# Optimization experiments

Hardware: AMD Instinct MI355X
Metric: run time of the kernel (lower is better)

The kernel has to match this reference:

```python
import jax, jax.numpy as jnp
import numpy as np

NUM_ITERS = 5
EPS = 1e-5


def setup_inputs() -> dict:
    key = jax.random.key(0)
    ks = jax.random.split(key, 5)
    C_in, C_out, D, H, W = 64, 64, 64, 256, 256
    return {
        "x": jax.random.normal(ks[0], (C_in, H, W), dtype=jnp.float32),
        "conv_w": jax.random.normal(ks[1], (C_out, C_in, 3, 3), dtype=jnp.float32) * 0.05,
        "conv_b": jax.random.normal(ks[2], (C_out,), dtype=jnp.float32) * 0.05,
        "bin_proj": jax.random.normal(ks[3], (C_out, D, 1), dtype=jnp.float32),
        "weight_matrix": jax.random.normal(ks[4], (C_out, D, D), dtype=jnp.float32),
        "gn_weight": jnp.ones((C_out,), dtype=jnp.float32),
        "gn_bias": jnp.zeros((C_out,), dtype=jnp.float32),
    }


def reference(x, conv_w, conv_b, bin_proj, weight_matrix, gn_weight, gn_bias):
    # query conv: (C_in,H,W) -> (C_out,H,W), SAME padding
    q = jax.lax.conv_general_dilated(
        x[None], conv_w, window_strides=(1, 1), padding="SAME",
        dimension_numbers=("NCHW", "OIHW", "NCHW"))[0]
    q = q + conv_b[:, None, None]

    bp = bin_proj[:, :, 0]  # (C, D) == bin_proj_c[:, 0] per channel
    # binary query / initial state: (C, H, W, D)
    state = jnp.sign(q[:, :, :, None] * bp[:, None, None, :])
    # unrolled Hopfield dynamics: state = sign(W_c @ state) per channel/pixel
    for _ in range(NUM_ITERS):
        state = jnp.sign(jnp.einsum("cde,chwe->chwd", weight_matrix, state))
    # readout: sum_d bp[c,d] * state[c,h,w,d] -> (C,H,W)
    out = jnp.einsum("cd,chwd->chw", bp, state)

    # GroupNorm(groups=1) over (C,H,W) with per-channel affine, then residual input is out+q
    y = out + q
    mean = jnp.mean(y)
    var = jnp.mean(jnp.square(y - mean))
    yn = (y - mean) * jax.lax.rsqrt(var + EPS)
    yn = yn * gn_weight[:, None, None] + gn_bias[:, None, None]
    return jax.nn.gelu(yn)
```

## Files before the change

kernel.cpp:

```cpp
#include <hip/hip_runtime.h>
#include <math.h>

#define N_TOT 4194304
#define CONV_BLOCKS 1024
#define XS_PAD 4864

__device__ __forceinline__ float sgnf(float x) {
    return x > 0.f ? 1.f : (x < 0.f ? -1.f : 0.f);
}

__device__ __forceinline__ float gelu_f(float v) {
    const float c0 = 0.7978845608028654f;
    float inner = c0 * fmaf(0.044715f * v, v * v, v);
    return 0.5f * v * (1.f + tanhf(inner));
}

__device__ __forceinline__ void gll4(const float* g, float* l) {
    __builtin_amdgcn_global_load_lds((const __attribute__((address_space(1))) void*)g,
                                     (__attribute__((address_space(3))) void*)l, 4, 0, 0);
}

__global__ __launch_bounds__(64) void alpha_kernel(const float* __restrict__ bp,
                                                   const float* __restrict__ Wm,
                                                   float* __restrict__ alpha) {
    const int c = blockIdx.x, d = threadIdx.x;
    __shared__ float v[64];
    float bpv = bp[c * 64 + d];
    v[d] = sgnf(bpv);
    __syncthreads();
    const float* row = Wm + c * 4096 + d * 64;
    for (int it = 0; it < 5; ++it) {
        float s = 0.f;
        #pragma unroll
        for (int e = 0; e < 64; ++e) s = fmaf(row[e], v[e], s);
        __syncthreads();
        v[d] = sgnf(s);
        __syncthreads();
    }
    float val = bpv * v[d];
    #pragma unroll
    for (int off = 32; off; off >>= 1) val += __shfl_down(val, off);
    if (d == 0) alpha[c] = val;
}

__global__ __launch_bounds__(256, 4) void conv_kernel(const float* __restrict__ x,
                                                      const float* __restrict__ cw,
                                                      const float* __restrict__ cb,
                                                      const float* __restrict__ alpha,
                                                      const float* __restrict__ zbuf,
                                                      float* __restrict__ y,
                                                      double* __restrict__ partials) {
    const int tid = threadIdx.x;
    const int b = blockIdx.x;
    const int tile = b & 63;
    const int cog = b >> 6;
    const int bx = tile & 7, by = tile >> 3;
    const int tx = tid & 15, ty = tid >> 4;
    const int x0 = (bx << 5) - 1, y0 = (by << 5) - 1;

    __shared__ float xs[2][XS_PAD];
    __shared__ double red[4][2];

    int voff[19];
    unsigned vmask = 0u;
    #pragma unroll
    for (int i = 0; i < 19; ++i) {
        int idx = i * 256 + tid;
        int r = idx / 136;
        int rem = idx - r * 136;
        int ci = rem / 34;
        int c = rem - ci * 34;
        int gy = y0 + r, gx = x0 + c;
        bool ok = (idx < 4624) && ((unsigned)gy < 256u) && ((unsigned)gx < 256u);
        voff[i] = (ci << 16) + (gy << 8) + gx;
        if (ok) vmask |= (1u << i);
    }

    float acc[4][2][2];
    #pragma unroll
    for (int co = 0; co < 4; ++co) {
        float bias = cb[cog * 4 + co];
        acc[co][0][0] = bias; acc[co][0][1] = bias;
        acc[co][1][0] = bias; acc[co][1][1] = bias;
    }

    #pragma unroll
    for (int i = 0; i < 19; ++i) {
        const float* src = (vmask & (1u << i)) ? (x + voff[i]) : zbuf;
        gll4(src, &xs[0][i * 256 + tid]);
    }
    __syncthreads();

    const int lrow = (2 * ty) * 136 + tx;
    const float* wbase = cw + cog * 4 * 576;

    for (int s = 0; s < 16; ++s) {
        const int cur = s & 1;
        if (s < 15) {
            const float* xb = x + ((s + 1) << 18);
            #pragma unroll
            for (int i = 0; i < 19; ++i) {
                const float* src = (vmask & (1u << i)) ? (xb + voff[i]) : zbuf;
                gll4(src, &xs[cur ^ 1][i * 256 + tid]);
            }
        }

        const float* xsc = xs[cur];
        #pragma unroll
        for (int ci = 0; ci < 4; ++ci) {
            float t[4][6];
            #pragma unroll
            for (int rr = 0; rr < 4; ++rr) {
                const int off = lrow + rr * 136 + ci * 34;
                t[rr][0] = xsc[off];      t[rr][1] = xsc[off + 1];  t[rr][2] = xsc[off + 2];
                t[rr][3] = xsc[off + 16]; t[rr][4] = xsc[off + 17]; t[rr][5] = xsc[off + 18];
            }
            const float* wp = wbase + ((s * 4 + ci) * 9);
            #pragma unroll
            for (int co = 0; co < 4; ++co) {
                const float* w = wp + co * 576;
                #pragma unroll
                for (int ky = 0; ky < 3; ++ky)
                    #pragma unroll
                    for (int kx = 0; kx < 3; ++kx) {
                        float wv = w[ky * 3 + kx];
                        #pragma unroll
                        for (int dy = 0; dy < 2; ++dy)
                            #pragma unroll
                            for (int g = 0; g < 2; ++g)
                                acc[co][dy][g] = fmaf(wv, t[dy + ky][g * 3 + kx], acc[co][dy][g]);
                    }
            }
        }
        __syncthreads();
    }

    double s1 = 0.0, s2 = 0.0;
    const int gx0 = (bx << 5) + tx;
    const int gy0 = (by << 5) + 2 * ty;
    #pragma unroll
    for (int co = 0; co < 4; ++co) {
        float a = alpha[cog * 4 + co];
        const int cb_off = (cog * 4 + co) << 16;
        #pragma unroll
        for (int dy = 0; dy < 2; ++dy) {
            #pragma unroll
            for (int g = 0; g < 2; ++g) {
                float q = acc[co][dy][g];
                float yv = q + (q > 0.f ? a : (q < 0.f ? -a : 0.f));
                y[cb_off + ((gy0 + dy) << 8) + gx0 + g * 16] = yv;
                s1 += (double)yv;
                s2 += (double)yv * (double)yv;
            }
        }
    }
    #pragma unroll
    for (int off = 32; off; off >>= 1) {
        s1 += __shfl_down(s1, off);
        s2 += __shfl_down(s2, off);
    }
    const int wid = tid >> 6;
    if ((tid & 63) == 0) { red[wid][0] = s1; red[wid][1] = s2; }
    __syncthreads();
    if (tid == 0) {
        double a1 = red[0][0] + red[1][0] + red[2][0] + red[3][0];
        double a2 = red[0][1] + red[1][1] + red[2][1] + red[3][1];
        partials[b * 2]     = a1;
        partials[b * 2 + 1] = a2;
    }
}

__global__ __launch_bounds__(256) void stats_kernel(const double* __restrict__ partials,
                                                    float* __restrict__ stats) {
    const int tid = threadIdx.x;
    double s1 = 0.0, s2 = 0.0;
    for (int i = tid; i < CONV_BLOCKS; i += 256) {
        s1 += partials[2 * i];
        s2 += partials[2 * i + 1];
    }
    #pragma unroll
    for (int off = 32; off; off >>= 1) {
        s1 += __shfl_down(s1, off);
        s2 += __shfl_down(s2, off);
    }
    __shared__ double red[4][2];
    const int wid = tid >> 6;
    if ((tid & 63) == 0) { red[wid][0] = s1; red[wid][1] = s2; }
    __syncthreads();
    if (tid == 0) {
        double a1 = red[0][0] + red[1][0] + red[2][0] + red[3][0];
        double a2 = red[0][1] + red[1][1] + red[2][1] + red[3][1];
        double mean = a1 / (double)N_TOT;
        double var = a2 / (double)N_TOT - mean * mean;
        stats[0] = (float)mean;
        stats[1] = (float)(1.0 / sqrt(var + 1e-5));
    }
}

__global__ __launch_bounds__(256) void finalize_kernel(float* __restrict__ y,
                                                       const float* __restrict__ stats,
                                                       const float* __restrict__ gnw,
                                                       const float* __restrict__ gnb) {
    const int i = blockIdx.x * 256 + threadIdx.x;
    const float mean = stats[0], istd = stats[1];
    const int c = i >> 14;
    const float scale = gnw[c] * istd;
    const float shift = gnb[c] - mean * scale;
    float4 v = reinterpret_cast<float4*>(y)[i];
    v.x = gelu_f(fmaf(v.x, scale, shift));
    v.y = gelu_f(fmaf(v.y, scale, shift));
    v.z = gelu_f(fmaf(v.z, scale, shift));
    v.w = gelu_f(fmaf(v.w, scale, shift));
    reinterpret_cast<float4*>(y)[i] = v;
}

extern "C" void kernel_launch(void* const* d_in, const int* in_sizes, int n_in,
                              void* d_out, int out_size, void* d_ws, size_t ws_size,
                              hipStream_t stream) {
    const float* x   = (const float*)d_in[0];
    const float* cw  = (const float*)d_in[1];
    const float* cb  = (const float*)d_in[2];
    const float* bp  = (const float*)d_in[3];
    const float* Wm  = (const float*)d_in[4];
    const float* gnw = (const float*)d_in[5];
    const float* gnb = (const float*)d_in[6];
    float* out = (float*)d_out;

    char* ws = (char*)d_ws;
    float* alpha     = (float*)ws;
    float* stats     = (float*)(ws + 256);
    double* partials = (double*)(ws + 512);
    float* zbuf      = (float*)(ws + 32768);

    hipMemsetAsync(zbuf, 0, 256, stream);
    alpha_kernel<<<64, 64, 0, stream>>>(bp, Wm, alpha);
    conv_kernel<<<CONV_BLOCKS, 256, 0, stream>>>(x, cw, cb, alpha, zbuf, out, partials);
    stats_kernel<<<1, 256, 0, stream>>>(partials, stats);
    finalize_kernel<<<4096, 256, 0, stream>>>(out, stats, gnw, gnb);
}
```

Baseline: 104.1 us.

## Remap conv thread tiles to 1x4 rows with vectorized LDS reads and stores

Result: slower. 150.4 us (+44.4%).

```diff
diff --git a/kernel.cpp b/kernel.cpp
--- a/kernel.cpp
+++ b/kernel.cpp
@@ -3,7 +3,7 @@
 
 #define N_TOT 4194304
 #define CONV_BLOCKS 1024
-#define XS_PAD 4864
+#define XS_DW 4896
 
 __device__ __forceinline__ float sgnf(float x) {
     return x > 0.f ? 1.f : (x < 0.f ? -1.f : 0.f);
@@ -55,10 +55,9 @@
     const int tile = b & 63;
     const int cog = b >> 6;
     const int bx = tile & 7, by = tile >> 3;
-    const int tx = tid & 15, ty = tid >> 4;
-    const int x0 = (bx << 5) - 1, y0 = (by << 5) - 1;
-
-    __shared__ float xs[2][XS_PAD];
+    const int tx = tid & 7, ty = tid >> 3;
+
+    __shared__ float xs[2][XS_DW];
     __shared__ double red[4][2];
 
     int voff[19];
@@ -66,56 +65,72 @@
     #pragma unroll
     for (int i = 0; i < 19; ++i) {
         int idx = i * 256 + tid;
-        int r = idx / 136;
-        int rem = idx - r * 136;
-        int ci = rem / 34;
-        int c = rem - ci * 34;
-        int gy = y0 + r, gx = x0 + c;
-        bool ok = (idx < 4624) && ((unsigned)gy < 256u) && ((unsigned)gx < 256u);
+        int r = idx / 144;
+        int rem = idx - r * 144;
+        int ci = rem / 36;
+        int cs = rem - ci * 36;
+        int gy = (by << 5) - 1 + r;
+        int gx = (bx << 5) + cs - 1;
+        bool ok = (cs < 34) && ((unsigned)gy < 256u) && ((unsigned)gx < 256u);
         voff[i] = (ci << 16) + (gy << 8) + gx;
         if (ok) vmask |= (1u << i);
     }
-
-    float acc[4][2][2];
+    int toff = 0; bool tok = false;
+    {
+        int cs = 4 + tid;
+        int gy = (by << 5) + 32;
+        int gx = (bx << 5) + cs - 1;
+        tok = (tid < 32) && (cs < 34) && (gy < 256) && ((unsigned)gx < 256u);
+        toff = (3 << 16) + (gy << 8) + gx;
+    }
+
+    float acc[4][4];
     #pragma unroll
     for (int co = 0; co < 4; ++co) {
         float bias = cb[cog * 4 + co];
-        acc[co][0][0] = bias; acc[co][0][1] = bias;
-        acc[co][1][0] = bias; acc[co][1][1] = bias;
-    }
-
-    #pragma unroll
-    for (int i = 0; i < 19; ++i) {
-        const float* src = (vmask & (1u << i)) ? (x + voff[i]) : zbuf;
-        gll4(src, &xs[0][i * 256 + tid]);
-    }
-    __syncthreads();
-
-    const int lrow = (2 * ty) * 136 + tx;
+        #pragma unroll
+        for (int j = 0; j < 4; ++j) acc[co][j] = bias;
+    }
+
+    {
+        float tv = tok ? x[toff] : 0.f;
+        #pragma unroll
+        for (int i = 0; i < 19; ++i) {
+            const float* src = (vmask & (1u << i)) ? (x + voff[i]) : zbuf;
+            gll4(src, &xs[0][i * 256 + tid]);
+        }
+        if (tid < 32) xs[0][4864 + tid] = tv;
+    }
+    __syncthreads();
+
     const float* wbase = cw + cog * 4 * 576;
 
     for (int s = 0; s < 16; ++s) {
         const int cur = s & 1;
         if (s < 15) {
             const float* xb = x + ((s + 1) << 18);
+            float tv = tok ? xb[toff] : 0.f;
             #pragma unroll
             for (int i = 0; i < 19; ++i) {
                 const float* src = (vmask & (1u << i)) ? (xb + voff[i]) : zbuf;
                 gll4(src, &xs[cur ^ 1][i * 256 + tid]);
             }
+            if (tid < 32) xs[cur ^ 1][4864 + tid] = tv;
         }
 
         const float* xsc = xs[cur];
         #pragma unroll
         for (int ci = 0; ci < 4; ++ci) {
-            float t[4][6];
+            float t[3][6];
             #pragma unroll
-            for (int rr = 0; rr < 4; ++rr) {
-                const int off = lrow + rr * 136 + ci * 34;
-                t[rr][0] = xsc[off];      t[rr][1] = xsc[off + 1];  t[rr][2] = xsc[off + 2];
-                t[rr][3] = xsc[off + 16]; t[rr][4] = xsc[off + 17]; t[rr][5] = xsc[off + 18];
+            for (int rr = 0; rr < 3; ++rr) {
+                const int base = (ty + rr) * 144 + ci * 36 + 4 * tx;
+                float4 a4 = *reinterpret_cast<const float4*>(&xsc[base]);
+                float2 a2 = *reinterpret_cast<const float2*>(&xsc[base + 4]);
+                t[rr][0] = a4.x; t[rr][1] = a4.y; t[rr][2] = a4.z; t[rr][3] = a4.w;
+                t[rr][4] = a2.x; t[rr][5] = a2.y;
             }
-            const float* wp = wbase + ((s * 4 + ci) * 9);
+            const float* wp = wbase + (s * 4 + ci) * 9;
             #pragma unroll
             for (int co = 0; co < 4; ++co) {
                 const float* w = wp + co * 576;
@@ -125,10 +140,8 @@
                     for (int kx = 0; kx < 3; ++kx) {
                         float wv = w[ky * 3 + kx];
                         #pragma unroll
-                        for (int dy = 0; dy < 2; ++dy)
-                            #pragma unroll
-                            for (int g = 0; g < 2; ++g)
-                                acc[co][dy][g] = fmaf(wv, t[dy + ky][g * 3 + kx], acc[co][dy][g]);
+                        for (int j = 0; j < 4; ++j)
+                            acc[co][j] = fmaf(wv, t[ky][kx + j], acc[co][j]);
                     }
             }
         }
@@ -136,23 +149,22 @@
     }
 
     double s1 = 0.0, s2 = 0.0;
-    const int gx0 = (bx << 5) + tx;
-    const int gy0 = (by << 5) + 2 * ty;
+    const int row = (by << 5) + ty;
+    const int col0 = (bx << 5) + 4 * tx;
     #pragma unroll
     for (int co = 0; co < 4; ++co) {
         float a = alpha[cog * 4 + co];
-        const int cb_off = (cog * 4 + co) << 16;
-        #pragma unroll
-        for (int dy = 0; dy < 2; ++dy) {
-            #pragma unroll
-            for (int g = 0; g < 2; ++g) {
-                float q = acc[co][dy][g];
-                float yv = q + (q > 0.f ? a : (q < 0.f ? -a : 0.f));
-                y[cb_off + ((gy0 + dy) << 8) + gx0 + g * 16] = yv;
-                s1 += (double)yv;
-                s2 += (double)yv * (double)yv;
-            }
-        }
+        float4 o;
+        float* op = &o.x;
+        #pragma unroll
+        for (int j = 0; j < 4; ++j) {
+            float q = acc[co][j];
+            float yv = q + (q > 0.f ? a : (q < 0.f ? -a : 0.f));
+            op[j] = yv;
+            s1 += (double)yv;
+            s2 += (double)yv * (double)yv;
+        }
+        *reinterpret_cast<float4*>(&y[((cog * 4 + co) << 16) + (row << 8) + col0]) = o;
     }
     #pragma unroll
     for (int off = 32; off; off >>= 1) {
```

## Stage conv weights in LDS and halve per-stage input channels

Applied to the files above, without the earlier changes.

After: 110.1 us. 5.7% more time.

```diff
diff --git a/kernel.cpp b/kernel.cpp
--- a/kernel.cpp
+++ b/kernel.cpp
@@ -3,7 +3,7 @@
 
 #define N_TOT 4194304
 #define CONV_BLOCKS 1024
-#define XS_PAD 4864
+#define XS_DW 2560
 
 __device__ __forceinline__ float sgnf(float x) {
     return x > 0.f ? 1.f : (x < 0.f ? -1.f : 0.f);
@@ -56,24 +56,34 @@
     const int cog = b >> 6;
     const int bx = tile & 7, by = tile >> 3;
     const int tx = tid & 15, ty = tid >> 4;
-    const int x0 = (bx << 5) - 1, y0 = (by << 5) - 1;
-
-    __shared__ float xs[2][XS_PAD];
+
+    __shared__ float xs[2][XS_DW];
+    __shared__ float wlds[2][128];
     __shared__ double red[4][2];
 
-    int voff[19];
+    int voff[10];
     unsigned vmask = 0u;
     #pragma unroll
-    for (int i = 0; i < 19; ++i) {
+    for (int i = 0; i < 10; ++i) {
         int idx = i * 256 + tid;
-        int r = idx / 136;
-        int rem = idx - r * 136;
-        int ci = rem / 34;
-        int c = rem - ci * 34;
-        int gy = y0 + r, gx = x0 + c;
-        bool ok = (idx < 4624) && ((unsigned)gy < 256u) && ((unsigned)gx < 256u);
+        int r = idx / 72;
+        int rem = idx - r * 72;
+        int ci = rem / 36;
+        int cs = rem - ci * 36;
+        int gy = (by << 5) - 1 + r;
+        int gx = (bx << 5) + cs - 1;
+        bool ok = (idx < 2448) && (cs < 34) && ((unsigned)gy < 256u) && ((unsigned)gx < 256u);
         voff[i] = (ci << 16) + (gy << 8) + gx;
         if (ok) vmask |= (1u << i);
+    }
+    int woff = 0; bool wok = false;
+    {
+        int wci = tid / 48;
+        int rem = tid - wci * 48;
+        int wco = rem / 12;
+        int wk = rem - wco * 12;
+        wok = (tid < 96) && (wk < 9);
+        woff = (cog * 4 + wco) * 576 + wci * 9 + wk;
     }
 
     float acc[4][2][2];
@@ -85,40 +95,51 @@
     }
 
     #pragma unroll
-    for (int i = 0; i < 19; ++i) {
+    for (int i = 0; i < 10; ++i) {
         const float* src = (vmask & (1u << i)) ? (x + voff[i]) : zbuf;
         gll4(src, &xs[0][i * 256 + tid]);
     }
-    __syncthreads();
-
-    const int lrow = (2 * ty) * 136 + tx;
-    const float* wbase = cw + cog * 4 * 576;
-
-    for (int s = 0; s < 16; ++s) {
+    if (tid < 128) {
+        const float* src = wok ? (cw + woff) : zbuf;
+        gll4(src, &wlds[0][tid]);
+    }
+    __syncthreads();
+
+    const int lbase = (2 * ty) * 72 + tx;
+
+    for (int s = 0; s < 32; ++s) {
         const int cur = s & 1;
-        if (s < 15) {
-            const float* xb = x + ((s + 1) << 18);
-            #pragma unroll
-            for (int i = 0; i < 19; ++i) {
+        if (s < 31) {
+            const float* xb = x + ((s + 1) << 17);
+            #pragma unroll
+            for (int i = 0; i < 10; ++i) {
                 const float* src = (vmask & (1u << i)) ? (xb + voff[i]) : zbuf;
                 gll4(src, &xs[cur ^ 1][i * 256 + tid]);
             }
+            if (tid < 128) {
+                const float* src = wok ? (cw + woff + (s + 1) * 18) : zbuf;
+                gll4(src, &wlds[cur ^ 1][tid]);
+            }
         }
 
         const float* xsc = xs[cur];
+        const float* wsc = wlds[cur];
         #pragma unroll
-        for (int ci = 0; ci < 4; ++ci) {
+        for (int ci = 0; ci < 2; ++ci) {
             float t[4][6];
             #pragma unroll
             for (int rr = 0; rr < 4; ++rr) {
-                const int off = lrow + rr * 136 + ci * 34;
+                const int off = lbase + rr * 72 + ci * 36;
                 t[rr][0] = xsc[off];      t[rr][1] = xsc[off + 1];  t[rr][2] = xsc[off + 2];
                 t[rr][3] = xsc[off + 16]; t[rr][4] = xsc[off + 17]; t[rr][5] = xsc[off + 18];
             }
-            const float* wp = wbase + ((s * 4 + ci) * 9);
             #pragma unroll
             for (int co = 0; co < 4; ++co) {
-                const float* w = wp + co * 576;
+                const int wb = ci * 48 + co * 12;
+                float4 wa = *reinterpret_cast<const float4*>(&wsc[wb]);
+                float4 wbv = *reinterpret_cast<const float4*>(&wsc[wb + 4]);
+                float  w8 = wsc[wb + 8];
+                const float w[9] = {wa.x, wa.y, wa.z, wa.w, wbv.x, wbv.y, wbv.z, wbv.w, w8};
                 #pragma unroll
                 for (int ky = 0; ky < 3; ++ky)
                     #pragma unroll
```
